# Kernel optimization log

Measured on AMD Instinct MI355X. Metric: run time of the kernel, lower is better.

Reference implementation:

```python
import jax, jax.numpy as jnp
import numpy as np

NEG_BIG = -1.0e9


def setup_inputs() -> dict:
    key = jax.random.key(0)
    kq, kk, kv, km = jax.random.split(key, 4)
    B, H, S, D = 8, 16, 1024, 64
    q = jax.random.normal(kq, (B, H, S, D), dtype=jnp.float32)
    k = jax.random.normal(kk, (B, H, S, D), dtype=jnp.float32)
    v = jax.random.normal(kv, (B, H, S, D), dtype=jnp.float32)
    mask = jax.random.uniform(km, (S - 1, S - 1), dtype=jnp.float32)
    return {"q": q, "k": k, "v": v, "mask": mask}


def reference(q, k, v, mask):
    # scores: [B,H,S,S]
    dk = k.shape[-1]
    logits = jnp.einsum("bhsd,bhtd->bhst", q, k) / jnp.sqrt(jnp.asarray(dk, q.dtype))
    if mask is not None:
        # original adds mask*-1e9 only on logits[:, :, 1:, 1:];
        # equivalent to padding mask with a zero first row/col then adding.
        mask_padded = jnp.pad(mask, ((1, 0), (1, 0)))  # [S, S]
        logits = logits + mask_padded * NEG_BIG
    attention_weights = jax.nn.softmax(logits, axis=-1)
    output = jnp.einsum("bhst,bhtd->bhsd", attention_weights, v)
    return (output, attention_weights)
```

## Files before the change

### kernel.cpp

```cpp
#include <hip/hip_runtime.h>

#define S_LEN 1024
#define D_DIM 64
#define QB 16
#define NTHREADS 1024
#define LSTR 1036
#define ESTR 2072
#define ELO 1024
#define RINV_OFF 66304
#define LDS_BYTES 66368

#define NBH 128
#define KV_ELEMS ((size_t)NBH * S_LEN * D_DIM)
#define WS_NEED (KV_ELEMS * 8)

typedef short s16x8 __attribute__((ext_vector_type(8)));
typedef short s16x4 __attribute__((ext_vector_type(4)));
typedef float f32x4 __attribute__((ext_vector_type(4)));
typedef unsigned short u16;
typedef unsigned int u32;

static __device__ __forceinline__ u16 f2bf_rne(float f) {
  u32 u = __builtin_bit_cast(u32, f);
  return (u16)((u + 0x7fffu + ((u >> 16) & 1u)) >> 16);
}

static __device__ __forceinline__ void split2(float f, u16& h, u16& l) {
  u32 u = __builtin_bit_cast(u32, f);
  h = (u16)(u >> 16);
  float hf = __builtin_bit_cast(float, u & 0xffff0000u);
  l = f2bf_rne(f - hf);
}

static __device__ __forceinline__ f32x4 mfma16(s16x8 a, s16x8 b, f32x4 c) {
  return __builtin_amdgcn_mfma_f32_16x16x32_bf16(a, b, c, 0, 0, 0);
}

static __device__ __forceinline__ void cvt8(f32x4 a, f32x4 b, s16x8& h, s16x8& l) {
  s16x8 hh, ll;
#pragma unroll
  for (int j = 0; j < 8; ++j) {
    float fj = (j < 4) ? a[j] : b[j - 4];
    u16 hb, lb;
    split2(fj, hb, lb);
    hh[j] = (short)hb;
    ll[j] = (short)lb;
  }
  h = hh; l = ll;
}

extern "C" __global__ void __launch_bounds__(256)
presplit_k(const float* __restrict__ kg, u16* __restrict__ khi, u16* __restrict__ klo) {
  const size_t base = ((size_t)blockIdx.x * 256 + threadIdx.x) * 8;
  f32x4 a = __builtin_nontemporal_load((const f32x4*)(kg + base));
  f32x4 b = __builtin_nontemporal_load((const f32x4*)(kg + base + 4));
  s16x8 h, l;
  cvt8(a, b, h, l);
  *(s16x8*)(khi + base) = h;
  *(s16x8*)(klo + base) = l;
}

extern "C" __global__ void __launch_bounds__(256)
presplit_vt(const float* __restrict__ vg, u16* __restrict__ vthi, u16* __restrict__ vtlo) {
  __shared__ u16 ht[64][72];
  __shared__ u16 lt[64][72];
  const int tid = threadIdx.x;
  const int bh = blockIdx.x >> 4;
  const int t0 = (blockIdx.x & 15) * 64;
  const float* vp = vg + ((size_t)bh * S_LEN + t0) * D_DIM;
#pragma unroll
  for (int it = 0; it < 16; ++it) {
    const int idx = it * 256 + tid;
    float f = __builtin_nontemporal_load(vp + idx);
    u16 h, l;
    split2(f, h, l);
    ht[idx & 63][idx >> 6] = h;
    lt[idx & 63][idx >> 6] = l;
  }
  __syncthreads();
#pragma unroll
  for (int o = tid; o < 2048; o += 256) {
    const int d = o >> 5;
    const int tp = (o & 31) * 2;
    u32 wh = (u32)ht[d][tp] | ((u32)ht[d][tp + 1] << 16);
    u32 wl = (u32)lt[d][tp] | ((u32)lt[d][tp + 1] << 16);
    const size_t off = ((size_t)bh * D_DIM + d) * S_LEN + t0 + tp;
    *(u32*)(vthi + off) = wh;
    *(u32*)(vtlo + off) = wl;
  }
}

template <bool PRE>
__global__ __launch_bounds__(NTHREADS, 8) void
attn_fused(const float* __restrict__ qg, const float* __restrict__ kg,
           const float* __restrict__ vg, const float* __restrict__ mg,
           float* __restrict__ og, float* __restrict__ wg,
           const u16* __restrict__ khi, const u16* __restrict__ klo,
           const u16* __restrict__ vthi, const u16* __restrict__ vtlo)
{
  extern __shared__ char smem[];
  float* L = (float*)smem;
  u16* E = (u16*)smem;
  float* sc = (float*)smem;
  float* rinv = (float*)(smem + RINV_OFF);

  const int tid = threadIdx.x;
  const int wave = tid >> 6;
  const int lane = tid & 63;
  const int l15 = lane & 15;
  const int lg4 = lane >> 4;

  const int bid = (int)blockIdx.x;
  const int swz = (bid & 7) * 1024 + (bid >> 3);
  const int qb = swz & 63;
  const int bh = swz >> 6;
  const int qbase = qb * QB;

  const float* qp = qg + (size_t)bh * S_LEN * D_DIM;

  {
    s16x8 qh[2], ql[2];
    const float* qrow = qp + (size_t)(qbase + l15) * D_DIM + lg4 * 8;
#pragma unroll
    for (int ks = 0; ks < 2; ++ks) {
      f32x4 a = *(const f32x4*)(qrow + ks * 32);
      f32x4 b = *(const f32x4*)(qrow + ks * 32 + 4);
#pragma unroll
      for (int j = 0; j < 4; ++j) { a[j] *= 0.125f; b[j] *= 0.125f; }
      cvt8(a, b, qh[ks], ql[ks]);
    }

#pragma unroll 2
    for (int ct = 0; ct < 4; ++ct) {
      const int t = wave * 64 + ct * 16 + l15;
      s16x8 kh[2], kl[2];
      if constexpr (PRE) {
        const u16* kb = khi + ((size_t)bh * S_LEN + t) * D_DIM + lg4 * 8;
        const u16* lb = klo + ((size_t)bh * S_LEN + t) * D_DIM + lg4 * 8;
#pragma unroll
        for (int ks = 0; ks < 2; ++ks) {
          kh[ks] = *(const s16x8*)(kb + ks * 32);
          kl[ks] = *(const s16x8*)(lb + ks * 32);
        }
      } else {
        const float* krow = kg + ((size_t)bh * S_LEN + t) * D_DIM + lg4 * 8;
#pragma unroll
        for (int ks = 0; ks < 2; ++ks) {
          f32x4 a = *(const f32x4*)(krow + ks * 32);
          f32x4 b = *(const f32x4*)(krow + ks * 32 + 4);
          cvt8(a, b, kh[ks], kl[ks]);
        }
      }
      f32x4 acc = {0.f, 0.f, 0.f, 0.f};
#pragma unroll
      for (int ks = 0; ks < 2; ++ks) {
        acc = mfma16(qh[ks], kh[ks], acc);
        acc = mfma16(qh[ks], kl[ks], acc);
        acc = mfma16(ql[ks], kh[ks], acc);
      }
#pragma unroll
      for (int j = 0; j < 4; ++j) {
        const int rl = lg4 * 4 + j;
        const int s = qbase + rl;
        float mv = 0.f;
        if (s > 0 && t > 0) mv = mg[(size_t)(s - 1) * (S_LEN - 1) + (t - 1)];
        L[rl * LSTR + t] = fmaf(mv, -1.0e9f, acc[j]);
      }
    }
  }
  __syncthreads();

  {
    const float* Lr = L + wave * LSTR;
    f32x4 lv[4];
#pragma unroll
    for (int g = 0; g < 4; ++g) lv[g] = *(const f32x4*)&Lr[lane * 4 + g * 256];
    float m = -3.402823466e38f;
#pragma unroll
    for (int g = 0; g < 4; ++g)
#pragma unroll
      for (int j = 0; j < 4; ++j) m = fmaxf(m, lv[g][j]);
#pragma unroll
    for (int off = 1; off < 64; off <<= 1) m = fmaxf(m, __shfl_xor(m, off, 64));

    float sum = 0.f;
#pragma unroll
    for (int g = 0; g < 4; ++g)
#pragma unroll
      for (int j = 0; j < 4; ++j) {
        float ex = __expf(lv[g][j] - m);
        lv[g][j] = ex;
        sum += ex;
      }
#pragma unroll
    for (int off = 1; off < 64; off <<= 1) sum += __shfl_xor(sum, off, 64);
    const float inv = 1.0f / sum;
    if (lane == 0) rinv[wave] = inv;

    float* wrow = wg + (size_t)bh * S_LEN * S_LEN + (size_t)(qbase + wave) * S_LEN;
    u16* Er = E + wave * ESTR;
#pragma unroll
    for (int g = 0; g < 4; ++g) {
      const int col = lane * 4 + g * 256;
      f32x4 wv;
      s16x4 eh, el;
#pragma unroll
      for (int j = 0; j < 4; ++j) {
        wv[j] = lv[g][j] * inv;
        u16 hb, lb;
        split2(lv[g][j], hb, lb);
        eh[j] = (short)hb;
        el[j] = (short)lb;
      }
      __builtin_nontemporal_store(wv, (f32x4*)&wrow[col]);
      *(s16x4*)&Er[col] = eh;
      *(s16x4*)&Er[ELO + col] = el;
    }
  }
  __syncthreads();

  const int g3 = wave >> 2;
  const int ct = wave & 3;
  const int dcol = ct * 16 + l15;
  f32x4 acc = {0.f, 0.f, 0.f, 0.f};
#pragma unroll 2
  for (int T = g3 * 8; T < g3 * 8 + 8; ++T) {
    const int t0 = T * 32 + lg4 * 8;
    s16x8 vh, vl;
    if constexpr (PRE) {
      const size_t off = ((size_t)bh * D_DIM + dcol) * S_LEN + t0;
      vh = *(const s16x8*)(vthi + off);
      vl = *(const s16x8*)(vtlo + off);
    } else {
#pragma unroll
      for (int i = 0; i < 8; ++i) {
        u16 hb, lb;
        split2(vg[((size_t)bh * S_LEN + t0 + i) * D_DIM + dcol], hb, lb);
        vh[i] = (short)hb;
        vl[i] = (short)lb;
      }
    }
    s16x8 ah = *(const s16x8*)&E[l15 * ESTR + t0];
    s16x8 al = *(const s16x8*)&E[l15 * ESTR + ELO + t0];
    acc = mfma16(ah, vh, acc);
    acc = mfma16(ah, vl, acc);
    acc = mfma16(al, vh, acc);
  }
  __syncthreads();

#pragma unroll
  for (int j = 0; j < 4; ++j)
    sc[g3 * 1024 + (lg4 * 4 + j) * 64 + dcol] = acc[j];
  __syncthreads();

  {
    const int q = wave;
    const int d = lane;
    float s = sc[q * 64 + d] + sc[1024 + q * 64 + d] +
              sc[2048 + q * 64 + d] + sc[3072 + q * 64 + d];
    __builtin_nontemporal_store(s * rinv[q],
        &og[(size_t)bh * S_LEN * D_DIM + (size_t)(qbase + q) * D_DIM + d]);
  }
}

extern "C" void kernel_launch(void* const* d_in, const int* in_sizes, int n_in,
                              void* d_out, int out_size, void* d_ws, size_t ws_size,
                              hipStream_t stream) {
  const float* q = (const float*)d_in[0];
  const float* k = (const float*)d_in[1];
  const float* v = (const float*)d_in[2];
  const float* m = (const float*)d_in[3];
  float* out = (float*)d_out;
  float* w = out + (size_t)8 * 16 * S_LEN * D_DIM;

  u16* khi = (u16*)d_ws;
  u16* klo = khi + KV_ELEMS;
  u16* vthi = klo + KV_ELEMS;
  u16* vtlo = vthi + KV_ELEMS;

  if (ws_size >= WS_NEED) {
    presplit_k<<<dim3(4096), 256, 0, stream>>>(k, khi, klo);
    presplit_vt<<<dim3(2048), 256, 0, stream>>>(v, vthi, vtlo);
    hipFuncSetAttribute(reinterpret_cast<const void*>(attn_fused<true>),
                        hipFuncAttributeMaxDynamicSharedMemorySize, LDS_BYTES);
    attn_fused<true><<<dim3(8192), NTHREADS, LDS_BYTES, stream>>>(
        q, k, v, m, out, w, khi, klo, vthi, vtlo);
  } else {
    hipFuncSetAttribute(reinterpret_cast<const void*>(attn_fused<false>),
                        hipFuncAttributeMaxDynamicSharedMemorySize, LDS_BYTES);
    attn_fused<false><<<dim3(8192), NTHREADS, LDS_BYTES, stream>>>(
        q, k, v, m, out, w, khi, klo, vthi, vtlo);
  }
}
```

Before: 1.092 ms.

## Defer attention-weight stores past PV matmul and reduce output with one fewer barrier

The attention-weight global stores move from the softmax phase to the end of the kernel. The weights are rebuilt from the bf16 hi/lo pairs already held in LDS, so the PV matmul no longer waits behind the large weight write. The PV partial-sum reduction now uses a separate LDS region. Wave group 0 adds the other groups' partials to its own registers, which removes one barrier. The cost is about 12KB more LDS per block, which may lower occupancy, and the stored weights are the hi+lo bf16 reconstruction (about 16 mantissa bits) rather than the exact fp32 values.

After: 1.134 ms. 1.04x slower.

```diff
diff --git a/kernel.cpp b/kernel.cpp
--- a/kernel.cpp
+++ b/kernel.cpp
@@ -8,7 +8,8 @@
 #define ESTR 2072
 #define ELO 1024
 #define RINV_OFF 66304
-#define LDS_BYTES 66368
+#define SC_OFF 66368
+#define LDS_BYTES 78656
 
 #define NBH 128
 #define KV_ELEMS ((size_t)NBH * S_LEN * D_DIM)
@@ -19,6 +20,10 @@
 typedef float f32x4 __attribute__((ext_vector_type(4)));
 typedef unsigned short u16;
 typedef unsigned int u32;
+
+static __device__ __forceinline__ float bf2f(u16 h) {
+  return __builtin_bit_cast(float, ((u32)h) << 16);
+}
 
 static __device__ __forceinline__ u16 f2bf_rne(float f) {
   u32 u = __builtin_bit_cast(u32, f);
@@ -101,8 +106,8 @@
   extern __shared__ char smem[];
   float* L = (float*)smem;
   u16* E = (u16*)smem;
-  float* sc = (float*)smem;
   float* rinv = (float*)(smem + RINV_OFF);
+  float* sc = (float*)(smem + SC_OFF);
 
   const int tid = threadIdx.x;
   const int wave = tid >> 6;
@@ -197,22 +202,18 @@
     const float inv = 1.0f / sum;
     if (lane == 0) rinv[wave] = inv;
 
-    float* wrow = wg + (size_t)bh * S_LEN * S_LEN + (size_t)(qbase + wave) * S_LEN;
     u16* Er = E + wave * ESTR;
 #pragma unroll
     for (int g = 0; g < 4; ++g) {
       const int col = lane * 4 + g * 256;
-      f32x4 wv;
       s16x4 eh, el;
 #pragma unroll
       for (int j = 0; j < 4; ++j) {
-        wv[j] = lv[g][j] * inv;
         u16 hb, lb;
         split2(lv[g][j], hb, lb);
         eh[j] = (short)hb;
         el[j] = (short)lb;
       }
-      __builtin_nontemporal_store(wv, (f32x4*)&wrow[col]);
       *(s16x4*)&Er[col] = eh;
       *(s16x4*)&Er[ELO + col] = el;
     }
@@ -246,20 +247,41 @@
     acc = mfma16(ah, vl, acc);
     acc = mfma16(al, vh, acc);
   }
+
+  if (g3 > 0) {
+#pragma unroll
+    for (int j = 0; j < 4; ++j)
+      sc[(g3 - 1) * 1024 + (lg4 * 4 + j) * 64 + dcol] = acc[j];
+  }
   __syncthreads();
 
-#pragma unroll
-  for (int j = 0; j < 4; ++j)
-    sc[g3 * 1024 + (lg4 * 4 + j) * 64 + dcol] = acc[j];
-  __syncthreads();
+  if (g3 == 0) {
+    float* op = og + (size_t)bh * S_LEN * D_DIM;
+#pragma unroll
+    for (int j = 0; j < 4; ++j) {
+      const int rl = lg4 * 4 + j;
+      float s = acc[j] + sc[rl * 64 + dcol] + sc[1024 + rl * 64 + dcol] +
+                sc[2048 + rl * 64 + dcol];
+      __builtin_nontemporal_store(s * rinv[rl],
+          &op[(size_t)(qbase + rl) * D_DIM + dcol]);
+    }
+  }
 
   {
-    const int q = wave;
-    const int d = lane;
-    float s = sc[q * 64 + d] + sc[1024 + q * 64 + d] +
-              sc[2048 + q * 64 + d] + sc[3072 + q * 64 + d];
-    __builtin_nontemporal_store(s * rinv[q],
-        &og[(size_t)bh * S_LEN * D_DIM + (size_t)(qbase + q) * D_DIM + d]);
+    const float winv = rinv[wave];
+    const u16* Er = E + wave * ESTR;
+    float* wrow = wg + (size_t)bh * S_LEN * S_LEN + (size_t)(qbase + wave) * S_LEN;
+#pragma unroll
+    for (int g = 0; g < 4; ++g) {
+      const int col = lane * 4 + g * 256;
+      s16x4 eh = *(const s16x4*)&Er[col];
+      s16x4 el = *(const s16x4*)&Er[ELO + col];
+      f32x4 wv;
+#pragma unroll
+      for (int j = 0; j < 4; ++j)
+        wv[j] = (bf2f((u16)eh[j]) + bf2f((u16)el[j])) * winv;
+      __builtin_nontemporal_store(wv, (f32x4*)&wrow[col]);
+    }
   }
 }
 
```
